# Performance work log

Hardware: AMD Instinct MI355X
Metric: run time of the kernel (lower is better)

## Reference

```python
import jax, jax.numpy as jnp
import numpy as np

N = 100000
E = 1600000
DIMS = [128, 128, 64]


def _gcn_norm(edge_index, num_nodes):
    # PyG gcn_norm: add self-loops, symmetric normalization D^-1/2 (A+I) D^-1/2
    src, dst = edge_index[0], edge_index[1]
    loop = jnp.arange(num_nodes, dtype=src.dtype)
    src = jnp.concatenate([src, loop])
    dst = jnp.concatenate([dst, loop])
    deg = jax.ops.segment_sum(jnp.ones_like(src, dtype=jnp.float32), dst,
                              num_segments=num_nodes)
    dinv = jnp.where(deg > 0, jax.lax.rsqrt(deg), 0.0)
    w = dinv[src] * dinv[dst]  # [E+N]
    return src, dst, w


def _gcn_conv(x, src, dst, w, W, b):
    # transform first (cheaper when out_dim <= in_dim), then aggregate
    h = x @ W                                   # [N, out]
    msg = h[src] * w[:, None]                   # gather + scale  [E+N, out]
    out = jax.ops.segment_sum(msg, dst, num_segments=x.shape[0])
    return out + b


def setup_inputs() -> dict:
    key = jax.random.key(0)
    ks = jax.random.split(key, 6)
    x = jax.random.normal(ks[0], (N, DIMS[0]), dtype=jnp.float32)
    edge_index = jax.random.randint(ks[1], (2, E), 0, N, dtype=jnp.int64)
    # Glorot-style init for GCNConv weights, zero bias (PyG default)
    W1 = jax.random.normal(ks[2], (DIMS[0], DIMS[1]), dtype=jnp.float32) / np.sqrt(DIMS[0])
    b1 = jnp.zeros((DIMS[1],), dtype=jnp.float32)
    W2 = jax.random.normal(ks[3], (DIMS[1], DIMS[2]), dtype=jnp.float32) / np.sqrt(DIMS[1])
    b2 = jnp.zeros((DIMS[2],), dtype=jnp.float32)
    return {"x": x, "edge_index": edge_index, "W1": W1, "b1": b1, "W2": W2, "b2": b2}


def reference(x, edge_index, W1, b1, W2, b2):
    src, dst, w = _gcn_norm(edge_index, x.shape[0])
    h = _gcn_conv(x, src, dst, w, W1, b1)
    h = jax.nn.relu(h)
    # dropout is identity in eval mode (deterministic reference)
    out = _gcn_conv(h, src, dst, w, W2, b2)
    return out
```

## Files before the change

### kernel.cpp

```cpp
#include <hip/hip_runtime.h>
#include <hip/hip_fp16.h>

#define TPB 256
#define CHUNK 1024
#define EPB 4096
#define CSHIFT 8

typedef _Float16 half8 __attribute__((ext_vector_type(8)));
typedef float    f32x4 __attribute__((ext_vector_type(4)));


__global__ __launch_bounds__(256) void scanA_kernel(const int* __restrict__ cnt,
                                                    int* __restrict__ row_ptr,
                                                    int* __restrict__ chunk_sums, int n) {
    __shared__ int ls[256];
    const int t    = threadIdx.x;
    const int base = blockIdx.x * CHUNK;
    const int idx  = base + t * 4;
    int4 v = make_int4(0, 0, 0, 0);
    if (idx + 3 < n) v = *(const int4*)(cnt + idx);
    else {
        if (idx + 0 < n) v.x = cnt[idx + 0];
        if (idx + 1 < n) v.y = cnt[idx + 1];
        if (idx + 2 < n) v.z = cnt[idx + 2];
        if (idx + 3 < n) v.w = cnt[idx + 3];
    }
    int s0 = v.x, s1 = s0 + v.y, s2 = s1 + v.z, s3 = s2 + v.w;
    ls[t] = s3;
    __syncthreads();
    for (int off = 1; off < 256; off <<= 1) {
        int xv = (t >= off) ? ls[t - off] : 0;
        __syncthreads();
        ls[t] += xv;
        __syncthreads();
    }
    int excl = (t == 0) ? 0 : ls[t - 1];
    if (idx + 0 < n) row_ptr[idx + 0] = excl;
    if (idx + 1 < n) row_ptr[idx + 1] = excl + s0;
    if (idx + 2 < n) row_ptr[idx + 2] = excl + s1;
    if (idx + 3 < n) row_ptr[idx + 3] = excl + s2;
    if (t == 255) chunk_sums[blockIdx.x] = ls[255];
}

__global__ __launch_bounds__(256) void scanB_kernel(int* __restrict__ chunk_sums, int nch) {
    __shared__ int ls[256];
    const int t = threadIdx.x;
    ls[t] = (t < nch) ? chunk_sums[t] : 0;
    __syncthreads();
    for (int off = 1; off < 256; off <<= 1) {
        int xv = (t >= off) ? ls[t - off] : 0;
        __syncthreads();
        ls[t] += xv;
        __syncthreads();
    }
    if (t < nch) chunk_sums[t] = (t == 0) ? 0 : ls[t - 1];
}

__global__ __launch_bounds__(256) void scanC_kernel(int* __restrict__ row_ptr,
                                                    const int* __restrict__ chunk_sums, int n) {
    const int base = blockIdx.x * CHUNK;
    const int off  = chunk_sums[blockIdx.x];
    for (int k = threadIdx.x; k < CHUNK; k += 256) {
        int i = base + k;
        if (i < n) row_ptr[i] += off;
    }
}


__global__ __launch_bounds__(256) void hist_kernel(const int* __restrict__ dst,
                                                   int* __restrict__ hist_g,
                                                   int e, int nbc, int nblk) {
    __shared__ int hs[512];
    const int t = threadIdx.x;
    for (int i = t; i < nbc; i += 256) hs[i] = 0;
    __syncthreads();
    const int e0  = blockIdx.x * EPB;
    const int lim = min(e0 + EPB, e);
    for (int i = e0 + t; i < lim; i += 256)
        atomicAdd(&hs[dst[i] >> CSHIFT], 1);
    __syncthreads();
    for (int b = t; b < nbc; b += 256)
        hist_g[b * nblk + blockIdx.x] = hs[b];
}

__global__ __launch_bounds__(256) void partition_kernel(const int* __restrict__ src,
                                                        const int* __restrict__ dst,
                                                        const int* __restrict__ hist_scan,
                                                        int* __restrict__ pairs,
                                                        int e, int nbc, int nblk) {
    __shared__ int  hs[512];
    __shared__ int  lscan[512];
    __shared__ int  lfill[512];
    __shared__ int  base_s[512];
    __shared__ int  ls[256];
    __shared__ int2 sp[EPB];
    const int t = threadIdx.x;
    for (int i = t; i < nbc; i += 256) { hs[i] = 0; lfill[i] = 0; }
    __syncthreads();
    const int e0  = blockIdx.x * EPB;
    const int lim = min(e0 + EPB, e);
    for (int i = e0 + t; i < lim; i += 256)
        atomicAdd(&hs[dst[i] >> CSHIFT], 1);
    __syncthreads();
    int v0 = (2 * t     < nbc) ? hs[2 * t]     : 0;
    int v1 = (2 * t + 1 < nbc) ? hs[2 * t + 1] : 0;
    ls[t] = v0 + v1;
    __syncthreads();
    for (int off = 1; off < 256; off <<= 1) {
        int xv = (t >= off) ? ls[t - off] : 0;
        __syncthreads();
        ls[t] += xv;
        __syncthreads();
    }
    int excl = (t == 0) ? 0 : ls[t - 1];
    if (2 * t     < nbc) lscan[2 * t]     = excl;
    if (2 * t + 1 < nbc) lscan[2 * t + 1] = excl + v0;
    for (int b = t; b < nbc; b += 256) base_s[b] = hist_scan[b * nblk + blockIdx.x];
    __syncthreads();
    for (int i = e0 + t; i < lim; i += 256) {
        int d = dst[i];
        int b = d >> CSHIFT;
        int r = atomicAdd(&lfill[b], 1);
        sp[lscan[b] + r] = make_int2(src[i], d);
    }
    __syncthreads();
    const int cnt = lim - e0;
    for (int i = t; i < cnt; i += 256) {
        int2 pr = sp[i];
        int  b  = pr.y >> CSHIFT;
        pairs[base_s[b] + (i - lscan[b])] = pr.x | ((pr.y & 255) << 17);
    }
}

__global__ __launch_bounds__(256) void bucket_finalize_kernel(const int* __restrict__ pairs,
                                                              const int* __restrict__ hist_scan,
                                                              int* __restrict__ row_ptr,
                                                              float* __restrict__ dinv,
                                                              int* __restrict__ csr_src,
                                                              int n, int e, int nbc, int nblk) {
    __shared__ int cnt_s[256];
    __shared__ int fill[256];
    __shared__ int ls[256];
    const int b   = blockIdx.x;
    const int nb0 = b << CSHIFT;
    const int t   = threadIdx.x;
    const int r0  = hist_scan[b * nblk];
    const int r1  = (b + 1 < nbc) ? hist_scan[(b + 1) * nblk] : e;
    cnt_s[t] = 0;
    __syncthreads();
    for (int i = r0 + t; i < r1; i += 256)
        atomicAdd(&cnt_s[pairs[i] >> 17], 1);
    __syncthreads();
    int c = cnt_s[t];
    ls[t] = c;
    __syncthreads();
    for (int off = 1; off < 256; off <<= 1) {
        int xv = (t >= off) ? ls[t - off] : 0;
        __syncthreads();
        ls[t] += xv;
        __syncthreads();
    }
    int excl = (t == 0) ? 0 : ls[t - 1];
    int node = nb0 + t;
    if (node < n) {
        row_ptr[node] = r0 + excl;
        dinv[node]    = rsqrtf((float)(c + 1));
    }
    fill[t] = r0 + excl;
    __syncthreads();
    for (int i = r0 + t; i < r1; i += 256) {
        int pr = pairs[i];
        int p  = atomicAdd(&fill[pr >> 17], 1);
        csr_src[p] = pr & 0x1FFFF;
    }
    if (b == 0 && t == 0) row_ptr[n] = e;
}


template <int M, bool RELU, typename XT>
__global__ __launch_bounds__(256) void gemm_mfma_kernel(const XT* __restrict__ X,
                                                        const float* __restrict__ W,
                                                        const float* __restrict__ dinv,
                                                        __half* __restrict__ H, int nrows) {
    constexpr int NC = M / 16;
    __shared__ __align__(16) _Float16 Wf[NC * 4 * 64 * 8];

    const int tid = threadIdx.x;

    for (int f = tid; f < NC * 4 * 64; f += 256) {
        int c    = f >> 8;
        int i    = (f >> 6) & 3;
        int lane = f & 63;
        int quad = lane >> 4, n = lane & 15;
        const float* wp = W + (size_t)(i * 32 + quad * 8) * M + c * 16 + n;
        half8 hv;
#pragma unroll
        for (int j = 0; j < 8; ++j) hv[j] = (_Float16)wp[(size_t)j * M];
        ((half8*)Wf)[f] = hv;
    }
    __syncthreads();

    const int  wave = tid >> 6, lane = tid & 63;
    const int  quad = lane >> 4, n16 = lane & 15;
    const long rowbase = (long)blockIdx.x * 64 + wave * 16;

    long arow = rowbase + n16;
    const XT* xrow = X + (size_t)(arow < nrows ? arow : 0) * 128;
    half8 a[4];
    if constexpr (sizeof(XT) == 4) {
        const float4* xr = (const float4*)xrow;
#pragma unroll
        for (int i = 0; i < 4; ++i) {
            float4 x0 = xr[i * 8 + quad * 2];
            float4 x1 = xr[i * 8 + quad * 2 + 1];
            if (RELU) {
                x0.x = fmaxf(x0.x, 0.f); x0.y = fmaxf(x0.y, 0.f);
                x0.z = fmaxf(x0.z, 0.f); x0.w = fmaxf(x0.w, 0.f);
                x1.x = fmaxf(x1.x, 0.f); x1.y = fmaxf(x1.y, 0.f);
                x1.z = fmaxf(x1.z, 0.f); x1.w = fmaxf(x1.w, 0.f);
            }
            half8 hv;
            hv[0] = (_Float16)x0.x; hv[1] = (_Float16)x0.y;
            hv[2] = (_Float16)x0.z; hv[3] = (_Float16)x0.w;
            hv[4] = (_Float16)x1.x; hv[5] = (_Float16)x1.y;
            hv[6] = (_Float16)x1.z; hv[7] = (_Float16)x1.w;
            a[i] = hv;
        }
    } else {
        const half8* xr = (const half8*)xrow;
#pragma unroll
        for (int i = 0; i < 4; ++i) {
            half8 hv = xr[i * 4 + quad];
            if (RELU) {
#pragma unroll
                for (int j = 0; j < 8; ++j)
                    hv[j] = (hv[j] > (_Float16)0) ? hv[j] : (_Float16)0;
            }
            a[i] = hv;
        }
    }

    float dv[4];
#pragma unroll
    for (int r = 0; r < 4; ++r) {
        long orow = rowbase + quad * 4 + r;
        dv[r] = (orow < nrows) ? dinv[orow] : 0.f;
    }

    for (int c = 0; c < NC; ++c) {
        f32x4 acc = {0.f, 0.f, 0.f, 0.f};
#pragma unroll
        for (int i = 0; i < 4; ++i) {
            half8 b = ((const half8*)Wf)[(c * 4 + i) * 64 + lane];
            acc = __builtin_amdgcn_mfma_f32_16x16x32_f16(a[i], b, acc, 0, 0, 0);
        }
#pragma unroll
        for (int r = 0; r < 4; ++r) {
            long orow = rowbase + quad * 4 + r;
            if (orow < nrows)
                H[orow * M + c * 16 + n16] = __float2half(acc[r] * dv[r]);
        }
    }
}


__device__ __forceinline__ void add_u4(float2* a, const uint4& u) {
    float2 v0 = __half22float2(*(const __half2*)&u.x);
    float2 v1 = __half22float2(*(const __half2*)&u.y);
    float2 v2 = __half22float2(*(const __half2*)&u.z);
    float2 v3 = __half22float2(*(const __half2*)&u.w);
    a[0].x += v0.x; a[0].y += v0.y;
    a[1].x += v1.x; a[1].y += v1.y;
    a[2].x += v2.x; a[2].y += v2.y;
    a[3].x += v3.x; a[3].y += v3.y;
}


__global__ __launch_bounds__(TPB) void agg_pull128_kernel(const __half* __restrict__ hs,
                                                          const int* __restrict__ csr_src,
                                                          const int* __restrict__ row_ptr,
                                                          const float* __restrict__ dinv,
                                                          const float* __restrict__ bias,
                                                          __half* __restrict__ out, int n) {
    const int node = blockIdx.x * (TPB / 64) + (threadIdx.x >> 6);
    const int lane = threadIdx.x & 63;
    if (node >= n) return;
    const int q  = lane >> 4;
    const int sl = lane & 15;
    const int beg = row_ptr[node];
    const int end = row_ptr[node + 1];
    const uint4* up = (const uint4*)hs;

    float2 a[4][4];
#pragma unroll
    for (int r = 0; r < 4; ++r)
#pragma unroll
        for (int k = 0; k < 4; ++k) a[r][k] = make_float2(0.f, 0.f);

    for (int base = beg; base < end; base += 64) {
        int m = end - base; if (m > 64) m = 64;
        int idx = (lane < m) ? csr_src[base + lane] : 0;
        for (int j = 0; j < m; j += 16) {
            int s0 = __shfl(idx, j + q);
            int s1 = __shfl(idx, j + 4 + q);
            int s2 = __shfl(idx, j + 8 + q);
            int s3 = __shfl(idx, j + 12 + q);
            uint4 u0 = up[(size_t)s0 * 16 + sl];
            uint4 u1 = up[(size_t)s1 * 16 + sl];
            uint4 u2 = up[(size_t)s2 * 16 + sl];
            uint4 u3 = up[(size_t)s3 * 16 + sl];
            if (j + q < m)      add_u4(a[0], u0);
            if (j + 4 + q < m)  add_u4(a[1], u1);
            if (j + 8 + q < m)  add_u4(a[2], u2);
            if (j + 12 + q < m) add_u4(a[3], u3);
        }
    }
#pragma unroll
    for (int k = 0; k < 4; ++k) {
        a[0][k].x += a[2][k].x; a[0][k].y += a[2][k].y;
        a[1][k].x += a[3][k].x; a[1][k].y += a[3][k].y;
        a[0][k].x += a[1][k].x; a[0][k].y += a[1][k].y;
    }
#pragma unroll
    for (int k = 0; k < 4; ++k) {
        a[0][k].x += __shfl(a[0][k].x, lane ^ 16);
        a[0][k].y += __shfl(a[0][k].y, lane ^ 16);
        a[0][k].x += __shfl(a[0][k].x, lane ^ 32);
        a[0][k].y += __shfl(a[0][k].y, lane ^ 32);
    }
    if (q == 0) {
        uint4 sv = up[(size_t)node * 16 + sl];
        float2 v0 = __half22float2(*(const __half2*)&sv.x);
        float2 v1 = __half22float2(*(const __half2*)&sv.y);
        float2 v2 = __half22float2(*(const __half2*)&sv.z);
        float2 v3 = __half22float2(*(const __half2*)&sv.w);
        float  di = dinv[node];
        const float4* bp = (const float4*)bias;
        float4 b0 = bp[2 * sl], b1 = bp[2 * sl + 1];
        __half2 h0 = __floats2half2_rn(b0.x + di * (a[0][0].x + v0.x),
                                       b0.y + di * (a[0][0].y + v0.y));
        __half2 h1 = __floats2half2_rn(b0.z + di * (a[0][1].x + v1.x),
                                       b0.w + di * (a[0][1].y + v1.y));
        __half2 h2 = __floats2half2_rn(b1.x + di * (a[0][2].x + v2.x),
                                       b1.y + di * (a[0][2].y + v2.y));
        __half2 h3 = __floats2half2_rn(b1.z + di * (a[0][3].x + v3.x),
                                       b1.w + di * (a[0][3].y + v3.y));
        uint4 ov;
        ov.x = *(const unsigned*)&h0; ov.y = *(const unsigned*)&h1;
        ov.z = *(const unsigned*)&h2; ov.w = *(const unsigned*)&h3;
        ((uint4*)out)[(size_t)node * 16 + sl] = ov;
    }
}


__global__ __launch_bounds__(TPB) void agg_pull64_kernel(const __half* __restrict__ hs,
                                                         const int* __restrict__ csr_src,
                                                         const int* __restrict__ row_ptr,
                                                         const float* __restrict__ dinv,
                                                         const float* __restrict__ bias,
                                                         float* __restrict__ out, int n) {
    const int node = blockIdx.x * (TPB / 64) + (threadIdx.x >> 6);
    const int lane = threadIdx.x & 63;
    if (node >= n) return;
    const int q  = lane >> 3;
    const int sl = lane & 7;
    const int beg = row_ptr[node];
    const int end = row_ptr[node + 1];
    const uint4* up = (const uint4*)hs;

    float2 a[2][4];
#pragma unroll
    for (int r = 0; r < 2; ++r)
#pragma unroll
        for (int k = 0; k < 4; ++k) a[r][k] = make_float2(0.f, 0.f);

    for (int base = beg; base < end; base += 64) {
        int m = end - base; if (m > 64) m = 64;
        int idx = (lane < m) ? csr_src[base + lane] : 0;
        for (int j = 0; j < m; j += 16) {
            int s0 = __shfl(idx, j + q);
            int s1 = __shfl(idx, j + 8 + q);
            uint4 u0 = up[(size_t)s0 * 8 + sl];
            uint4 u1 = up[(size_t)s1 * 8 + sl];
            if (j + q < m)     add_u4(a[0], u0);
            if (j + 8 + q < m) add_u4(a[1], u1);
        }
    }
#pragma unroll
    for (int k = 0; k < 4; ++k) {
        a[0][k].x += a[1][k].x; a[0][k].y += a[1][k].y;
    }
#pragma unroll
    for (int k = 0; k < 4; ++k) {
        a[0][k].x += __shfl(a[0][k].x, lane ^ 8);
        a[0][k].y += __shfl(a[0][k].y, lane ^ 8);
        a[0][k].x += __shfl(a[0][k].x, lane ^ 16);
        a[0][k].y += __shfl(a[0][k].y, lane ^ 16);
        a[0][k].x += __shfl(a[0][k].x, lane ^ 32);
        a[0][k].y += __shfl(a[0][k].y, lane ^ 32);
    }
    if (q == 0) {
        uint4 sv = up[(size_t)node * 8 + sl];
        float2 v0 = __half22float2(*(const __half2*)&sv.x);
        float2 v1 = __half22float2(*(const __half2*)&sv.y);
        float2 v2 = __half22float2(*(const __half2*)&sv.z);
        float2 v3 = __half22float2(*(const __half2*)&sv.w);
        float  di = dinv[node];
        const float4* bp = (const float4*)bias;
        float4 b0 = bp[2 * sl], b1 = bp[2 * sl + 1];
        float4 o0, o1;
        o0.x = b0.x + di * (a[0][0].x + v0.x);
        o0.y = b0.y + di * (a[0][0].y + v0.y);
        o0.z = b0.z + di * (a[0][1].x + v1.x);
        o0.w = b0.w + di * (a[0][1].y + v1.y);
        o1.x = b1.x + di * (a[0][2].x + v2.x);
        o1.y = b1.y + di * (a[0][2].y + v2.y);
        o1.z = b1.z + di * (a[0][3].x + v3.x);
        o1.w = b1.w + di * (a[0][3].y + v3.y);
        ((float4*)out)[(size_t)node * 16 + 2 * sl]     = o0;
        ((float4*)out)[(size_t)node * 16 + 2 * sl + 1] = o1;
    }
}


extern "C" void kernel_launch(void* const* d_in, const int* in_sizes, int n_in,
                              void* d_out, int out_size, void* d_ws, size_t ws_size,
                              hipStream_t stream) {
    const float* x  = (const float*)d_in[0];
    const int*   ei = (const int*)d_in[1];
    const float* W1 = (const float*)d_in[2];
    const float* b1 = (const float*)d_in[3];
    const float* W2 = (const float*)d_in[4];
    const float* b2 = (const float*)d_in[5];
    float* out = (float*)d_out;

    const int N = in_sizes[0] / 128;
    const int E = in_sizes[1] / 2;
    const int* srcv = ei;
    const int* dstv = ei + E;

    const int NBC    = (N + 255) >> CSHIFT;
    const int NBLK_E = (E + EPB - 1) / EPB;
    const int HLEN   = NBC * NBLK_E;
    const int NCHH   = (HLEN + CHUNK - 1) / CHUNK;

    char* p = (char*)d_ws;
    int*    row_ptr    = (int*)p;    p += (((size_t)N + 64) * 4 + 63) & ~(size_t)63;
    int*    chunk_sums = (int*)p;    p += 1024;
    int*    hist       = (int*)p;    p += (((size_t)HLEN + 64) * 4 + 63) & ~(size_t)63;
    int*    csr_src    = (int*)p;    p += ((size_t)E * 4 + 63) & ~(size_t)63;
    float*  dinv       = (float*)p;  p += (((size_t)N + 64) * 4 + 63) & ~(size_t)63;
    __half* hs1        = (__half*)p; p += (size_t)N * 128 * 2;
    __half* out1       = (__half*)p; p += (size_t)N * 128 * 2;
    int*    pairs      = (int*)out1;
    __half* hs2        = hs1;

    hist_kernel<<<NBLK_E, 256, 0, stream>>>(dstv, hist, E, NBC, NBLK_E);
    scanA_kernel<<<NCHH, 256, 0, stream>>>(hist, hist, chunk_sums, HLEN);
    scanB_kernel<<<1, 256, 0, stream>>>(chunk_sums, NCHH);
    scanC_kernel<<<NCHH, 256, 0, stream>>>(hist, chunk_sums, HLEN);
    partition_kernel<<<NBLK_E, 256, 0, stream>>>(srcv, dstv, hist, pairs, E, NBC, NBLK_E);
    bucket_finalize_kernel<<<NBC, 256, 0, stream>>>(pairs, hist, row_ptr, dinv, csr_src,
                                                    N, E, NBC, NBLK_E);

    gemm_mfma_kernel<128, false, float><<<(N + 63) / 64, 256, 0, stream>>>(x, W1, dinv, hs1, N);
    agg_pull128_kernel<<<(N + 3) / 4, TPB, 0, stream>>>(hs1, csr_src, row_ptr, dinv, b1, out1, N);

    gemm_mfma_kernel<64, true, _Float16><<<(N + 63) / 64, 256, 0, stream>>>(
        (const _Float16*)out1, W2, dinv, hs2, N);
    agg_pull64_kernel<<<(N + 3) / 4, TPB, 0, stream>>>(hs2, csr_src, row_ptr, dinv, b2, out, N);
}
```

Measured before the change: 291.3 us.

## Make aggregation kernels persistent with software-pipelined row metadata prefetch

Both pull-aggregation kernels now run a fixed grid of 2048 blocks, and each wavefront loops over nodes with a grid stride instead of owning one node. Row pointers for the node two steps ahead, plus the neighbour indices, self row and dinv for the next node, are loaded while the current node is being aggregated. This hides the dependent latency chain of row_ptr, csr_src and the feature gathers. The change also hoists the bias loads out of the node loop, cuts the accumulators from four row sets to two, and adds a fast path with no per-lane masking for full groups of 16 edges. In exchange the wavefront count is fixed and registers are held across iterations, which could reduce latency hiding from occupancy or cause load imbalance on high-degree nodes.

```diff
diff --git a/kernel.cpp b/kernel.cpp
--- a/kernel.cpp
+++ b/kernel.cpp
@@ -5,6 +5,7 @@
 #define CHUNK 1024
 #define EPB 4096
 #define CSHIFT 8
+#define AGG_BLOCKS 2048
 
 typedef _Float16 half8 __attribute__((ext_vector_type(8)));
 typedef float    f32x4 __attribute__((ext_vector_type(4)));
@@ -282,73 +283,95 @@
                                                           const float* __restrict__ dinv,
                                                           const float* __restrict__ bias,
                                                           __half* __restrict__ out, int n) {
-    const int node = blockIdx.x * (TPB / 64) + (threadIdx.x >> 6);
+    const int wid  = blockIdx.x * (TPB / 64) + (threadIdx.x >> 6);
+    const int NW   = gridDim.x * (TPB / 64);
     const int lane = threadIdx.x & 63;
-    if (node >= n) return;
-    const int q  = lane >> 4;
-    const int sl = lane & 15;
-    const int beg = row_ptr[node];
-    const int end = row_ptr[node + 1];
-    const uint4* up = (const uint4*)hs;
-
-    float2 a[4][4];
-#pragma unroll
-    for (int r = 0; r < 4; ++r)
-#pragma unroll
-        for (int k = 0; k < 4; ++k) a[r][k] = make_float2(0.f, 0.f);
-
-    for (int base = beg; base < end; base += 64) {
-        int m = end - base; if (m > 64) m = 64;
-        int idx = (lane < m) ? csr_src[base + lane] : 0;
-        for (int j = 0; j < m; j += 16) {
-            int s0 = __shfl(idx, j + q);
-            int s1 = __shfl(idx, j + 4 + q);
-            int s2 = __shfl(idx, j + 8 + q);
-            int s3 = __shfl(idx, j + 12 + q);
-            uint4 u0 = up[(size_t)s0 * 16 + sl];
-            uint4 u1 = up[(size_t)s1 * 16 + sl];
-            uint4 u2 = up[(size_t)s2 * 16 + sl];
-            uint4 u3 = up[(size_t)s3 * 16 + sl];
-            if (j + q < m)      add_u4(a[0], u0);
-            if (j + 4 + q < m)  add_u4(a[1], u1);
-            if (j + 8 + q < m)  add_u4(a[2], u2);
-            if (j + 12 + q < m) add_u4(a[3], u3);
-        }
-    }
-#pragma unroll
-    for (int k = 0; k < 4; ++k) {
-        a[0][k].x += a[2][k].x; a[0][k].y += a[2][k].y;
-        a[1][k].x += a[3][k].x; a[1][k].y += a[3][k].y;
-        a[0][k].x += a[1][k].x; a[0][k].y += a[1][k].y;
-    }
-#pragma unroll
-    for (int k = 0; k < 4; ++k) {
-        a[0][k].x += __shfl(a[0][k].x, lane ^ 16);
-        a[0][k].y += __shfl(a[0][k].y, lane ^ 16);
-        a[0][k].x += __shfl(a[0][k].x, lane ^ 32);
-        a[0][k].y += __shfl(a[0][k].y, lane ^ 32);
-    }
-    if (q == 0) {
-        uint4 sv = up[(size_t)node * 16 + sl];
-        float2 v0 = __half22float2(*(const __half2*)&sv.x);
-        float2 v1 = __half22float2(*(const __half2*)&sv.y);
-        float2 v2 = __half22float2(*(const __half2*)&sv.z);
-        float2 v3 = __half22float2(*(const __half2*)&sv.w);
-        float  di = dinv[node];
-        const float4* bp = (const float4*)bias;
-        float4 b0 = bp[2 * sl], b1 = bp[2 * sl + 1];
-        __half2 h0 = __floats2half2_rn(b0.x + di * (a[0][0].x + v0.x),
-                                       b0.y + di * (a[0][0].y + v0.y));
-        __half2 h1 = __floats2half2_rn(b0.z + di * (a[0][1].x + v1.x),
-                                       b0.w + di * (a[0][1].y + v1.y));
-        __half2 h2 = __floats2half2_rn(b1.x + di * (a[0][2].x + v2.x),
-                                       b1.y + di * (a[0][2].y + v2.y));
-        __half2 h3 = __floats2half2_rn(b1.z + di * (a[0][3].x + v3.x),
-                                       b1.w + di * (a[0][3].y + v3.y));
-        uint4 ov;
-        ov.x = *(const unsigned*)&h0; ov.y = *(const unsigned*)&h1;
-        ov.z = *(const unsigned*)&h2; ov.w = *(const unsigned*)&h3;
-        ((uint4*)out)[(size_t)node * 16 + sl] = ov;
+    const int q    = lane >> 4;
+    const int sl   = lane & 15;
+    if (wid >= n) return;
+    const uint4* up   = (const uint4*)hs;
+    const uint4* upsl = up + sl;
+
+    const float4* bp = (const float4*)bias;
+    const float4 bb0 = bp[2 * sl], bb1 = bp[2 * sl + 1];
+
+    int b0 = row_ptr[wid], e0 = row_ptr[wid + 1];
+    int nA = wid + NW;
+    int b1 = 0, e1 = 0;
+    if (nA < n) { b1 = row_ptr[nA]; e1 = row_ptr[nA + 1]; }
+    int m0 = e0 - b0; if (m0 > 64) m0 = 64;
+    int idx0 = (lane < m0) ? csr_src[b0 + lane] : 0;
+    uint4 self0 = make_uint4(0, 0, 0, 0);
+    if (q == 0) self0 = up[(size_t)wid * 16 + sl];
+    float dv0 = dinv[wid];
+
+    for (int ni = wid; ni < n; ni += NW) {
+        const int n1 = ni + NW, n2 = ni + 2 * NW;
+        int b2 = 0, e2 = 0;
+        if (n2 < n) { b2 = row_ptr[n2]; e2 = row_ptr[n2 + 1]; }
+        int idx1 = 0; uint4 self1 = make_uint4(0, 0, 0, 0); float dv1 = 0.f;
+        if (n1 < n) {
+            int m1 = e1 - b1; if (m1 > 64) m1 = 64;
+            idx1 = (lane < m1) ? csr_src[b1 + lane] : 0;
+            if (q == 0) self1 = up[(size_t)n1 * 16 + sl];
+            dv1 = dinv[n1];
+        }
+        float2 a0[4], a1[4];
+#pragma unroll
+        for (int k = 0; k < 4; ++k) { a0[k] = make_float2(0.f, 0.f); a1[k] = make_float2(0.f, 0.f); }
+        for (int base = b0; base < e0; base += 64) {
+            int m = e0 - base; if (m > 64) m = 64;
+            int idxv;
+            if (base == b0) idxv = idx0;
+            else            idxv = (lane < m) ? csr_src[base + lane] : 0;
+            for (int j = 0; j < m; j += 16) {
+                int s0 = __shfl(idxv, j + q);
+                int s1 = __shfl(idxv, j + 4 + q);
+                int s2 = __shfl(idxv, j + 8 + q);
+                int s3 = __shfl(idxv, j + 12 + q);
+                uint4 u0 = upsl[(size_t)(unsigned)s0 * 16];
+                uint4 u1 = upsl[(size_t)(unsigned)s1 * 16];
+                uint4 u2 = upsl[(size_t)(unsigned)s2 * 16];
+                uint4 u3 = upsl[(size_t)(unsigned)s3 * 16];
+                if (j + 16 <= m) {
+                    add_u4(a0, u0); add_u4(a1, u1); add_u4(a0, u2); add_u4(a1, u3);
+                } else {
+                    if (j + q < m)      add_u4(a0, u0);
+                    if (j + 4 + q < m)  add_u4(a1, u1);
+                    if (j + 8 + q < m)  add_u4(a0, u2);
+                    if (j + 12 + q < m) add_u4(a1, u3);
+                }
+            }
+        }
+#pragma unroll
+        for (int k = 0; k < 4; ++k) { a0[k].x += a1[k].x; a0[k].y += a1[k].y; }
+#pragma unroll
+        for (int k = 0; k < 4; ++k) {
+            a0[k].x += __shfl(a0[k].x, lane ^ 16);
+            a0[k].y += __shfl(a0[k].y, lane ^ 16);
+            a0[k].x += __shfl(a0[k].x, lane ^ 32);
+            a0[k].y += __shfl(a0[k].y, lane ^ 32);
+        }
+        if (q == 0) {
+            float2 v0 = __half22float2(*(const __half2*)&self0.x);
+            float2 v1 = __half22float2(*(const __half2*)&self0.y);
+            float2 v2 = __half22float2(*(const __half2*)&self0.z);
+            float2 v3 = __half22float2(*(const __half2*)&self0.w);
+            __half2 h0 = __floats2half2_rn(bb0.x + dv0 * (a0[0].x + v0.x),
+                                           bb0.y + dv0 * (a0[0].y + v0.y));
+            __half2 h1 = __floats2half2_rn(bb0.z + dv0 * (a0[1].x + v1.x),
+                                           bb0.w + dv0 * (a0[1].y + v1.y));
+            __half2 h2 = __floats2half2_rn(bb1.x + dv0 * (a0[2].x + v2.x),
+                                           bb1.y + dv0 * (a0[2].y + v2.y));
+            __half2 h3 = __floats2half2_rn(bb1.z + dv0 * (a0[3].x + v3.x),
+                                           bb1.w + dv0 * (a0[3].y + v3.y));
+            uint4 ov;
+            ov.x = *(const unsigned*)&h0; ov.y = *(const unsigned*)&h1;
+            ov.z = *(const unsigned*)&h2; ov.w = *(const unsigned*)&h3;
+            ((uint4*)out)[(size_t)ni * 16 + sl] = ov;
+        }
+        b0 = b1; e0 = e1; idx0 = idx1; self0 = self1; dv0 = dv1;
+        b1 = b2; e1 = e2;
     }
 }
 
@@ -359,66 +382,90 @@
                                                          const float* __restrict__ dinv,
                                                          const float* __restrict__ bias,
                                                          float* __restrict__ out, int n) {
-    const int node = blockIdx.x * (TPB / 64) + (threadIdx.x >> 6);
+    const int wid  = blockIdx.x * (TPB / 64) + (threadIdx.x >> 6);
+    const int NW   = gridDim.x * (TPB / 64);
     const int lane = threadIdx.x & 63;
-    if (node >= n) return;
-    const int q  = lane >> 3;
-    const int sl = lane & 7;
-    const int beg = row_ptr[node];
-    const int end = row_ptr[node + 1];
-    const uint4* up = (const uint4*)hs;
-
-    float2 a[2][4];
-#pragma unroll
-    for (int r = 0; r < 2; ++r)
-#pragma unroll
-        for (int k = 0; k < 4; ++k) a[r][k] = make_float2(0.f, 0.f);
-
-    for (int base = beg; base < end; base += 64) {
-        int m = end - base; if (m > 64) m = 64;
-        int idx = (lane < m) ? csr_src[base + lane] : 0;
-        for (int j = 0; j < m; j += 16) {
-            int s0 = __shfl(idx, j + q);
-            int s1 = __shfl(idx, j + 8 + q);
-            uint4 u0 = up[(size_t)s0 * 8 + sl];
-            uint4 u1 = up[(size_t)s1 * 8 + sl];
-            if (j + q < m)     add_u4(a[0], u0);
-            if (j + 8 + q < m) add_u4(a[1], u1);
-        }
-    }
-#pragma unroll
-    for (int k = 0; k < 4; ++k) {
-        a[0][k].x += a[1][k].x; a[0][k].y += a[1][k].y;
-    }
-#pragma unroll
-    for (int k = 0; k < 4; ++k) {
-        a[0][k].x += __shfl(a[0][k].x, lane ^ 8);
-        a[0][k].y += __shfl(a[0][k].y, lane ^ 8);
-        a[0][k].x += __shfl(a[0][k].x, lane ^ 16);
-        a[0][k].y += __shfl(a[0][k].y, lane ^ 16);
-        a[0][k].x += __shfl(a[0][k].x, lane ^ 32);
-        a[0][k].y += __shfl(a[0][k].y, lane ^ 32);
-    }
-    if (q == 0) {
-        uint4 sv = up[(size_t)node * 8 + sl];
-        float2 v0 = __half22float2(*(const __half2*)&sv.x);
-        float2 v1 = __half22float2(*(const __half2*)&sv.y);
-        float2 v2 = __half22float2(*(const __half2*)&sv.z);
-        float2 v3 = __half22float2(*(const __half2*)&sv.w);
-        float  di = dinv[node];
-        const float4* bp = (const float4*)bias;
-        float4 b0 = bp[2 * sl], b1 = bp[2 * sl + 1];
-        float4 o0, o1;
-        o0.x = b0.x + di * (a[0][0].x + v0.x);
-        o0.y = b0.y + di * (a[0][0].y + v0.y);
-        o0.z = b0.z + di * (a[0][1].x + v1.x);
-        o0.w = b0.w + di * (a[0][1].y + v1.y);
-        o1.x = b1.x + di * (a[0][2].x + v2.x);
-        o1.y = b1.y + di * (a[0][2].y + v2.y);
-        o1.z = b1.z + di * (a[0][3].x + v3.x);
-        o1.w = b1.w + di * (a[0][3].y + v3.y);
-        ((float4*)out)[(size_t)node * 16 + 2 * sl]     = o0;
-        ((float4*)out)[(size_t)node * 16 + 2 * sl + 1] = o1;
+    const int q    = lane >> 3;
+    const int sl   = lane & 7;
+    if (wid >= n) return;
+    const uint4* up   = (const uint4*)hs;
+    const uint4* upsl = up + sl;
+
+    const float4* bp = (const float4*)bias;
+    const float4 bb0 = bp[2 * sl], bb1 = bp[2 * sl + 1];
+
+    int b0 = row_ptr[wid], e0 = row_ptr[wid + 1];
+    int nA = wid + NW;
+    int b1 = 0, e1 = 0;
+    if (nA < n) { b1 = row_ptr[nA]; e1 = row_ptr[nA + 1]; }
+    int m0 = e0 - b0; if (m0 > 64) m0 = 64;
+    int idx0 = (lane < m0) ? csr_src[b0 + lane] : 0;
+    uint4 self0 = make_uint4(0, 0, 0, 0);
+    if (q == 0) self0 = up[(size_t)wid * 8 + sl];
+    float dv0 = dinv[wid];
+
+    for (int ni = wid; ni < n; ni += NW) {
+        const int n1 = ni + NW, n2 = ni + 2 * NW;
+        int b2 = 0, e2 = 0;
+        if (n2 < n) { b2 = row_ptr[n2]; e2 = row_ptr[n2 + 1]; }
+        int idx1 = 0; uint4 self1 = make_uint4(0, 0, 0, 0); float dv1 = 0.f;
+        if (n1 < n) {
+            int m1 = e1 - b1; if (m1 > 64) m1 = 64;
+            idx1 = (lane < m1) ? csr_src[b1 + lane] : 0;
+            if (q == 0) self1 = up[(size_t)n1 * 8 + sl];
+            dv1 = dinv[n1];
+        }
+        float2 a0[4], a1[4];
+#pragma unroll
+        for (int k = 0; k < 4; ++k) { a0[k] = make_float2(0.f, 0.f); a1[k] = make_float2(0.f, 0.f); }
+        for (int base = b0; base < e0; base += 64) {
+            int m = e0 - base; if (m > 64) m = 64;
+            int idxv;
+            if (base == b0) idxv = idx0;
+            else            idxv = (lane < m) ? csr_src[base + lane] : 0;
+            for (int j = 0; j < m; j += 16) {
+                int s0 = __shfl(idxv, j + q);
+                int s1 = __shfl(idxv, j + 8 + q);
+                uint4 u0 = upsl[(size_t)(unsigned)s0 * 8];
+                uint4 u1 = upsl[(size_t)(unsigned)s1 * 8];
+                if (j + 16 <= m) {
+                    add_u4(a0, u0); add_u4(a1, u1);
+                } else {
+                    if (j + q < m)     add_u4(a0, u0);
+                    if (j + 8 + q < m) add_u4(a1, u1);
+                }
+            }
+        }
+#pragma unroll
+        for (int k = 0; k < 4; ++k) { a0[k].x += a1[k].x; a0[k].y += a1[k].y; }
+#pragma unroll
+        for (int k = 0; k < 4; ++k) {
+            a0[k].x += __shfl(a0[k].x, lane ^ 8);
+            a0[k].y += __shfl(a0[k].y, lane ^ 8);
+            a0[k].x += __shfl(a0[k].x, lane ^ 16);
+            a0[k].y += __shfl(a0[k].y, lane ^ 16);
+            a0[k].x += __shfl(a0[k].x, lane ^ 32);
+            a0[k].y += __shfl(a0[k].y, lane ^ 32);
+        }
+        if (q == 0) {
+            float2 v0 = __half22float2(*(const __half2*)&self0.x);
+            float2 v1 = __half22float2(*(const __half2*)&self0.y);
+            float2 v2 = __half22float2(*(const __half2*)&self0.z);
+            float2 v3 = __half22float2(*(const __half2*)&self0.w);
+            float4 o0, o1;
+            o0.x = bb0.x + dv0 * (a0[0].x + v0.x);
+            o0.y = bb0.y + dv0 * (a0[0].y + v0.y);
+            o0.z = bb0.z + dv0 * (a0[1].x + v1.x);
+            o0.w = bb0.w + dv0 * (a0[1].y + v1.y);
+            o1.x = bb1.x + dv0 * (a0[2].x + v2.x);
+            o1.y = bb1.y + dv0 * (a0[2].y + v2.y);
+            o1.z = bb1.z + dv0 * (a0[3].x + v3.x);
+            o1.w = bb1.w + dv0 * (a0[3].y + v3.y);
+            ((float4*)out)[(size_t)ni * 16 + 2 * sl]     = o0;
+            ((float4*)out)[(size_t)ni * 16 + 2 * sl + 1] = o1;
+        }
+        b0 = b1; e0 = e1; idx0 = idx1; self0 = self1; dv0 = dv1;
+        b1 = b2; e1 = e2;
     }
 }
 
@@ -464,9 +511,9 @@
                                                     N, E, NBC, NBLK_E);
 
     gemm_mfma_kernel<128, false, float><<<(N + 63) / 64, 256, 0, stream>>>(x, W1, dinv, hs1, N);
-    agg_pull128_kernel<<<(N + 3) / 4, TPB, 0, stream>>>(hs1, csr_src, row_ptr, dinv, b1, out1, N);
+    agg_pull128_kernel<<<AGG_BLOCKS, TPB, 0, stream>>>(hs1, csr_src, row_ptr, dinv, b1, out1, N);
 
     gemm_mfma_kernel<64, true, _Float16><<<(N + 63) / 64, 256, 0, stream>>>(
         (const _Float16*)out1, W2, dinv, hs2, N);
-    agg_pull64_kernel<<<(N + 3) / 4, TPB, 0, stream>>>(hs2, csr_src, row_ptr, dinv, b2, out, N);
-}
+    agg_pull64_kernel<<<AGG_BLOCKS, TPB, 0, stream>>>(hs2, csr_src, row_ptr, dinv, b2, out, N);
+}
```

After: 282.9 us. -2.9%, faster.
